# Kernel tuning notes

Hardware: AMD Instinct MI355X
Metric: run time of the kernel (lower is better)

The kernel has to match this reference:

```python
import jax, jax.numpy as jnp
import numpy as np

B, T, H, V = 64, 512, 300, 50257


def setup_inputs() -> dict:
    key = jax.random.key(0)
    k0, k1, k2, k3, k4 = jax.random.split(key, 5)
    tokens = jax.random.randint(k0, (B, T), 0, V, dtype=jnp.int32)
    ihs = jnp.zeros((B, H), jnp.float32)
    emb = jax.random.normal(k1, (V, H), jnp.float32) * 0.02
    W = jax.random.normal(k2, (H, H), jnp.float32) * (1.0 / np.sqrt(H))
    U = jax.random.normal(k3, (H, H), jnp.float32) * (1.0 / np.sqrt(H))
    Wout = jax.random.normal(k4, (V, H), jnp.float32) * 0.02
    bout = jnp.zeros((V,), jnp.float32)
    return {"ihs": ihs, "tokens": tokens, "emb": emb, "W": W, "U": U,
            "Wout": Wout, "bout": bout}


def reference(ihs, tokens, emb, W, U, Wout, bout):
    # Embedding lookup: [B, T, H]
    x = emb[tokens]
    # Precompute input projection for all timesteps: U x_t (Linear: x @ U^T)
    ux = jnp.einsum('bth,gh->btg', x, U)  # [B, T, H]
    ux_tmajor = jnp.swapaxes(ux, 0, 1)    # [T, B, H]

    def step(h, ux_t):
        # h_t = tanh(W h_{t-1} + U x_t)
        h_next = jnp.tanh(h @ W.T + ux_t)
        return h_next, h_next

    h_last, _ = jax.lax.scan(step, ihs, ux_tmajor)
    # final hidden state -> vocab logits
    logits = h_last @ Wout.T + bout  # [B, V]
    return logits
```

## Files before the change

### kernel.cpp

```cpp
#include <hip/hip_runtime.h>
#include <math.h>

#define H 300
#define BB 64
#define TT 512
#define VV 50257
#define KC 30

typedef float v2f __attribute__((ext_vector_type(2)));

__global__ void transpose_k(const float* __restrict__ in, float* __restrict__ out) {
    int idx = blockIdx.x * blockDim.x + threadIdx.x;
    if (idx < H * H) {
        int r = idx / H, c = idx - r * H;
        out[idx] = in[c * H + r];
    }
}

__global__ __launch_bounds__(256) void ux_k(const int* __restrict__ tokens,
                                            const float* __restrict__ emb,
                                            const float* __restrict__ Ut,
                                            float* __restrict__ ux) {
    __shared__ __align__(16) float x_s[KC][BB];
    __shared__ __align__(16) float ut_s[KC][304];
    __shared__ int tok_s[BB];

    const int t = blockIdx.x;
    const int tid = threadIdx.x;
    if (tid < BB) tok_s[tid] = tokens[tid * TT + t];

    const int tb = tid >> 4;
    const int tg = tid & 15;
    const int b0 = tb * 4;
    const int g0 = tg * 20;
    const bool active = (tg < 15);

    v2f acc[4][10];
#pragma unroll
    for (int i = 0; i < 4; ++i)
#pragma unroll
        for (int j = 0; j < 10; ++j) acc[i][j] = (v2f){0.f, 0.f};

    __syncthreads();

    for (int h0 = 0; h0 < H; h0 += KC) {
        for (int i = tid; i < BB * 32; i += 256) {
            int b = i >> 5, k = i & 31;
            if (k < KC) x_s[k][b] = emb[tok_s[b] * H + h0 + k];
        }
        for (int i = tid; i < KC * H; i += 256) {
            int k = i / H, g = i - k * H;
            ut_s[k][g] = Ut[(h0 + k) * H + g];
        }
        __syncthreads();
        if (active) {
#pragma unroll 2
            for (int k = 0; k < KC; ++k) {
                float4 xa = *reinterpret_cast<const float4*>(&x_s[k][b0]);
                float4 u0 = *reinterpret_cast<const float4*>(&ut_s[k][g0 + 0]);
                float4 u1 = *reinterpret_cast<const float4*>(&ut_s[k][g0 + 4]);
                float4 u2 = *reinterpret_cast<const float4*>(&ut_s[k][g0 + 8]);
                float4 u3 = *reinterpret_cast<const float4*>(&ut_s[k][g0 + 12]);
                float4 u4 = *reinterpret_cast<const float4*>(&ut_s[k][g0 + 16]);
                const float xr[4] = {xa.x, xa.y, xa.z, xa.w};
                const v2f ur[10] = {{u0.x, u0.y}, {u0.z, u0.w},
                                    {u1.x, u1.y}, {u1.z, u1.w},
                                    {u2.x, u2.y}, {u2.z, u2.w},
                                    {u3.x, u3.y}, {u3.z, u3.w},
                                    {u4.x, u4.y}, {u4.z, u4.w}};
#pragma unroll
                for (int i = 0; i < 4; ++i) {
                    const v2f xs = {xr[i], xr[i]};
#pragma unroll
                    for (int j = 0; j < 10; ++j)
                        acc[i][j] = __builtin_elementwise_fma(xs, ur[j], acc[i][j]);
                }
            }
        }
        __syncthreads();
    }

    if (active) {
#pragma unroll
        for (int i = 0; i < 4; ++i) {
            float* dst = ux + (t * BB + b0 + i) * H + g0;
#pragma unroll
            for (int jq = 0; jq < 5; ++jq) {
                *reinterpret_cast<float4*>(dst + jq * 4) =
                    make_float4(acc[i][2 * jq].x, acc[i][2 * jq].y,
                                acc[i][2 * jq + 1].x, acc[i][2 * jq + 1].y);
            }
        }
    }
}

#define RNN_Q15(X) X(0) X(1) X(2) X(3) X(4) X(5) X(6) X(7) X(8) X(9) \
    X(10) X(11) X(12) X(13) X(14)

__global__ __attribute__((amdgpu_flat_work_group_size(768, 768), amdgpu_waves_per_eu(3, 3)))
void rnn_k(const float* __restrict__ W,
           const float* __restrict__ ux,
           const float* __restrict__ ihs,
           float* __restrict__ hlast) {
    __shared__ __align__(16) float shpool[20800];
    float* h_s = shpool;
    float* p_s = shpool + 304;

    const int b = blockIdx.x;
    const int tid = threadIdx.x;
    const int tt = (tid < 750) ? tid : 749;
    const int c  = tt / 150;
    const int g2 = tt - c * 150;

    const float4* w0p = reinterpret_cast<const float4*>(W + (size_t)(g2      ) * H + c * 60);
    const float4* w1p = reinterpret_cast<const float4*>(W + (size_t)(g2 + 150) * H + c * 60);

#define RNN_DW(q) \
    float4 t0_##q = w0p[q]; \
    v2f w0l_##q = {t0_##q.x, t0_##q.y}; v2f w0h_##q = {t0_##q.z, t0_##q.w}; \
    float4 t1_##q = w1p[q]; \
    v2f w1l_##q = {t1_##q.x, t1_##q.y}; v2f w1h_##q = {t1_##q.z, t1_##q.w};
    RNN_Q15(RNN_DW)
#undef RNN_DW

    if (tid < H) h_s[tid] = ihs[b * H + tid];

    const float* uxr = ux + (size_t)b * H + tid;
    float u = 0.f;
    if (tid < H) u = uxr[0];
    __syncthreads();

    const float4* hs4 = reinterpret_cast<const float4*>(h_s);
    const int c15 = c * 15;

#pragma unroll 1
    for (int t = 0; t < TT; ++t) {
        float n = 0.f;
        if (tid < H && t + 1 < TT)
            n = uxr[(size_t)(t + 1) * (BB * H)];
        v2f a0l = {0.f, 0.f}, a0h = {0.f, 0.f};
        v2f a1l = {0.f, 0.f}, a1h = {0.f, 0.f};
#define RNN_FMA(q) { float4 h4 = hs4[c15 + q]; \
        v2f hl = {h4.x, h4.y}; v2f hh = {h4.z, h4.w}; \
        a0l = __builtin_elementwise_fma(w0l_##q, hl, a0l); \
        a0h = __builtin_elementwise_fma(w0h_##q, hh, a0h); \
        a1l = __builtin_elementwise_fma(w1l_##q, hl, a1l); \
        a1h = __builtin_elementwise_fma(w1h_##q, hh, a1h); }
        RNN_Q15(RNN_FMA)
#undef RNN_FMA
        float pA = (a0l.x + a0l.y) + (a0h.x + a0h.y);
        float pB = (a1l.x + a1l.y) + (a1h.x + a1h.y);
        if (tid < 750) {
            p_s[c * 304 + g2      ] = pA;
            p_s[c * 304 + g2 + 150] = pB;
        }
        __syncthreads();
        if (tid < H) {
            float z = p_s[tid] + u;
            z += p_s[304 + tid];
            z += p_s[608 + tid];
            z += p_s[912 + tid];
            z += p_s[1216 + tid];
            float e = __expf(2.f * z);
            h_s[tid] = 1.f - 2.f * __builtin_amdgcn_rcpf(e + 1.f);
        }
        u = n;
        __syncthreads();
    }
    if (tid < H) hlast[b * H + tid] = h_s[tid];
}

__global__ __launch_bounds__(256) void logits_k(const float* __restrict__ hlast,
                                                const float* __restrict__ Wout,
                                                const float* __restrict__ bout,
                                                float* __restrict__ out) {
    __shared__ __align__(16) float Ws[32 * 132];
    __shared__ __align__(16) float hs[32 * 76];
    const int tid = threadIdx.x;
    const int tv = tid & 31;
    const int tb = tid >> 5;
    const int v0 = blockIdx.x * 128;

    float acc[8][4];
#pragma unroll
    for (int i = 0; i < 8; ++i)
#pragma unroll
        for (int j = 0; j < 4; ++j) acc[i][j] = 0.f;

    for (int hb = 0; hb < H; hb += 32) {
        __syncthreads();
        {
            const int vp = tid >> 1;
            const int hloc = (tid & 1) * 16;
            int vv = v0 + vp; if (vv > VV - 1) vv = VV - 1;
            const float* wrow = Wout + (size_t)vv * H + hb + hloc;
#pragma unroll
            for (int i = 0; i < 4; ++i) {
                const int hg = hb + hloc + i * 4;
                float4 val;
                if (hg + 3 < H) {
                    val = *reinterpret_cast<const float4*>(wrow + i * 4);
                } else {
                    val.x = (hg + 0 < H) ? wrow[i * 4 + 0] : 0.f;
                    val.y = (hg + 1 < H) ? wrow[i * 4 + 1] : 0.f;
                    val.z = (hg + 2 < H) ? wrow[i * 4 + 2] : 0.f;
                    val.w = (hg + 3 < H) ? wrow[i * 4 + 3] : 0.f;
                }
                Ws[(hloc + i * 4 + 0) * 132 + vp] = val.x;
                Ws[(hloc + i * 4 + 1) * 132 + vp] = val.y;
                Ws[(hloc + i * 4 + 2) * 132 + vp] = val.z;
                Ws[(hloc + i * 4 + 3) * 132 + vp] = val.w;
            }
        }
        {
            const int bb = tid >> 2;
            const int hl = (tid & 3) * 8;
            const float* hrow = hlast + bb * H + hb + hl;
#pragma unroll
            for (int i = 0; i < 2; ++i) {
                const int hg = hb + hl + i * 4;
                float4 val;
                if (hg + 3 < H) {
                    val = *reinterpret_cast<const float4*>(hrow + i * 4);
                } else {
                    val.x = (hg + 0 < H) ? hrow[i * 4 + 0] : 0.f;
                    val.y = (hg + 1 < H) ? hrow[i * 4 + 1] : 0.f;
                    val.z = (hg + 2 < H) ? hrow[i * 4 + 2] : 0.f;
                    val.w = (hg + 3 < H) ? hrow[i * 4 + 3] : 0.f;
                }
                hs[(hl + i * 4 + 0) * 76 + bb] = val.x;
                hs[(hl + i * 4 + 1) * 76 + bb] = val.y;
                hs[(hl + i * 4 + 2) * 76 + bb] = val.z;
                hs[(hl + i * 4 + 3) * 76 + bb] = val.w;
            }
        }
        __syncthreads();
        const float4* Ws4 = reinterpret_cast<const float4*>(Ws);
        const float4* hs4 = reinterpret_cast<const float4*>(hs);
#pragma unroll
        for (int h2 = 0; h2 < 32; ++h2) {
            float4 w4  = Ws4[h2 * 33 + tv];
            float4 h4a = hs4[h2 * 19 + tb * 2];
            float4 h4b = hs4[h2 * 19 + tb * 2 + 1];
            const float hv[8] = {h4a.x, h4a.y, h4a.z, h4a.w,
                                 h4b.x, h4b.y, h4b.z, h4b.w};
#pragma unroll
            for (int bi = 0; bi < 8; ++bi) {
                acc[bi][0] += hv[bi] * w4.x;
                acc[bi][1] += hv[bi] * w4.y;
                acc[bi][2] += hv[bi] * w4.z;
                acc[bi][3] += hv[bi] * w4.w;
            }
        }
    }

    const int vg = v0 + tv * 4;
    float4 bq;
    if (vg + 3 < VV) bq = *reinterpret_cast<const float4*>(bout + vg);
    else {
        bq.x = (vg + 0 < VV) ? bout[vg + 0] : 0.f;
        bq.y = (vg + 1 < VV) ? bout[vg + 1] : 0.f;
        bq.z = (vg + 2 < VV) ? bout[vg + 2] : 0.f;
        bq.w = (vg + 3 < VV) ? bout[vg + 3] : 0.f;
    }
#pragma unroll
    for (int bi = 0; bi < 8; ++bi) {
        const int bb = tb * 8 + bi;
        float* op = out + (size_t)bb * VV + vg;
        if (vg + 0 < VV) op[0] = acc[bi][0] + bq.x;
        if (vg + 1 < VV) op[1] = acc[bi][1] + bq.y;
        if (vg + 2 < VV) op[2] = acc[bi][2] + bq.z;
        if (vg + 3 < VV) op[3] = acc[bi][3] + bq.w;
    }
}

extern "C" void kernel_launch(void* const* d_in, const int* in_sizes, int n_in,
                              void* d_out, int out_size, void* d_ws, size_t ws_size,
                              hipStream_t stream) {
    const float* ihs    = (const float*)d_in[0];
    const int*   tokens = (const int*)  d_in[1];
    const float* emb    = (const float*)d_in[2];
    const float* W      = (const float*)d_in[3];
    const float* U      = (const float*)d_in[4];
    const float* Wout   = (const float*)d_in[5];
    const float* bout   = (const float*)d_in[6];
    float* out = (float*)d_out;

    char* ws = (char*)d_ws;
    float* Ut    = (float*)(ws + 0);
    float* hlast = (float*)(ws + 400000);
    float* ux    = (float*)(ws + 1048576);

    const int tp_blocks = (H * H + 255) / 256;
    transpose_k<<<tp_blocks, 256, 0, stream>>>(U, Ut);
    ux_k<<<TT, 256, 0, stream>>>(tokens, emb, Ut, ux);
    rnn_k<<<BB, 768, 0, stream>>>(W, ux, ihs, hlast);
    logits_k<<<(VV + 127) / 128, 256, 0, stream>>>(hlast, Wout, bout, out);
}
```

Measured before the change: 705.8 us.

## Split RNN recurrence into four chunked launches and pack logits FMAs

The serial RNN kernel now runs over 128-step chunks, launched four times in sequence. Each launch carries the hidden state through a workspace buffer, read in place by the same block that writes it. Separately, the logits kernel accumulates into 2-wide vectors with elementwise FMA so the compiler can emit packed FP32 FMAs. The chunking adds three launches and reloads W into registers each time, with no clear speed benefit. The packed FMA targets the ALU cost of the logits GEMM.

```diff
diff --git a/kernel.cpp b/kernel.cpp
--- a/kernel.cpp
+++ b/kernel.cpp
@@ -6,6 +6,7 @@
 #define TT 512
 #define VV 50257
 #define KC 30
+#define TCHUNK 128
 
 typedef float v2f __attribute__((ext_vector_type(2)));
 
@@ -100,8 +101,9 @@
 __global__ __attribute__((amdgpu_flat_work_group_size(768, 768), amdgpu_waves_per_eu(3, 3)))
 void rnn_k(const float* __restrict__ W,
            const float* __restrict__ ux,
-           const float* __restrict__ ihs,
-           float* __restrict__ hlast) {
+           const float* __restrict__ hin,
+           float* __restrict__ hout,
+           int t0) {
     __shared__ __align__(16) float shpool[20800];
     float* h_s = shpool;
     float* p_s = shpool + 304;
@@ -123,18 +125,18 @@
     RNN_Q15(RNN_DW)
 #undef RNN_DW
 
-    if (tid < H) h_s[tid] = ihs[b * H + tid];
+    if (tid < H) h_s[tid] = hin[b * H + tid];
 
     const float* uxr = ux + (size_t)b * H + tid;
     float u = 0.f;
-    if (tid < H) u = uxr[0];
+    if (tid < H) u = uxr[(size_t)t0 * (BB * H)];
     __syncthreads();
 
     const float4* hs4 = reinterpret_cast<const float4*>(h_s);
     const int c15 = c * 15;
 
 #pragma unroll 1
-    for (int t = 0; t < TT; ++t) {
+    for (int t = t0; t < t0 + TCHUNK; ++t) {
         float n = 0.f;
         if (tid < H && t + 1 < TT)
             n = uxr[(size_t)(t + 1) * (BB * H)];
@@ -167,7 +169,7 @@
         u = n;
         __syncthreads();
     }
-    if (tid < H) hlast[b * H + tid] = h_s[tid];
+    if (tid < H) hout[b * H + tid] = h_s[tid];
 }
 
 __global__ __launch_bounds__(256) void logits_k(const float* __restrict__ hlast,
@@ -181,11 +183,12 @@
     const int tb = tid >> 5;
     const int v0 = blockIdx.x * 128;
 
-    float acc[8][4];
-#pragma unroll
-    for (int i = 0; i < 8; ++i)
-#pragma unroll
-        for (int j = 0; j < 4; ++j) acc[i][j] = 0.f;
+    v2f acc[8][2];
+#pragma unroll
+    for (int i = 0; i < 8; ++i) {
+        acc[i][0] = (v2f){0.f, 0.f};
+        acc[i][1] = (v2f){0.f, 0.f};
+    }
 
     for (int hb = 0; hb < H; hb += 32) {
         __syncthreads();
@@ -242,14 +245,15 @@
             float4 w4  = Ws4[h2 * 33 + tv];
             float4 h4a = hs4[h2 * 19 + tb * 2];
             float4 h4b = hs4[h2 * 19 + tb * 2 + 1];
+            const v2f wl = {w4.x, w4.y};
+            const v2f wh = {w4.z, w4.w};
             const float hv[8] = {h4a.x, h4a.y, h4a.z, h4a.w,
                                  h4b.x, h4b.y, h4b.z, h4b.w};
 #pragma unroll
             for (int bi = 0; bi < 8; ++bi) {
-                acc[bi][0] += hv[bi] * w4.x;
-                acc[bi][1] += hv[bi] * w4.y;
-                acc[bi][2] += hv[bi] * w4.z;
-                acc[bi][3] += hv[bi] * w4.w;
+                const v2f hb2 = {hv[bi], hv[bi]};
+                acc[bi][0] = __builtin_elementwise_fma(hb2, wl, acc[bi][0]);
+                acc[bi][1] = __builtin_elementwise_fma(hb2, wh, acc[bi][1]);
             }
         }
     }
@@ -267,10 +271,10 @@
     for (int bi = 0; bi < 8; ++bi) {
         const int bb = tb * 8 + bi;
         float* op = out + (size_t)bb * VV + vg;
-        if (vg + 0 < VV) op[0] = acc[bi][0] + bq.x;
-        if (vg + 1 < VV) op[1] = acc[bi][1] + bq.y;
-        if (vg + 2 < VV) op[2] = acc[bi][2] + bq.z;
-        if (vg + 3 < VV) op[3] = acc[bi][3] + bq.w;
+        if (vg + 0 < VV) op[0] = acc[bi][0].x + bq.x;
+        if (vg + 1 < VV) op[1] = acc[bi][0].y + bq.y;
+        if (vg + 2 < VV) op[2] = acc[bi][1].x + bq.z;
+        if (vg + 3 < VV) op[3] = acc[bi][1].y + bq.w;
     }
 }
 
@@ -287,13 +291,16 @@
     float* out = (float*)d_out;
 
     char* ws = (char*)d_ws;
-    float* Ut    = (float*)(ws + 0);
-    float* hlast = (float*)(ws + 400000);
-    float* ux    = (float*)(ws + 1048576);
+    float* Ut     = (float*)(ws + 0);
+    float* hstate = (float*)(ws + 400000);
+    float* ux     = (float*)(ws + 1048576);
 
     const int tp_blocks = (H * H + 255) / 256;
     transpose_k<<<tp_blocks, 256, 0, stream>>>(U, Ut);
     ux_k<<<TT, 256, 0, stream>>>(tokens, emb, Ut, ux);
-    rnn_k<<<BB, 768, 0, stream>>>(W, ux, ihs, hlast);
-    logits_k<<<(VV + 127) / 128, 256, 0, stream>>>(hlast, Wout, bout, out);
-}
+    rnn_k<<<BB, 768, 0, stream>>>(W, ux, ihs,    hstate, 0);
+    rnn_k<<<BB, 768, 0, stream>>>(W, ux, hstate, hstate, 128);
+    rnn_k<<<BB, 768, 0, stream>>>(W, ux, hstate, hstate, 256);
+    rnn_k<<<BB, 768, 0, stream>>>(W, ux, hstate, hstate, 384);
+    logits_k<<<(VV + 127) / 128, 256, 0, stream>>>(hstate, Wout, bout, out);
+}
```

New measurement: 719.8 us. No clear change (+2.0%).
